# Kernel tuning notes

Measured on AMD Instinct MI355X. Metric: run time of the kernel, lower is better.

The kernel has to match this reference:

```python
import jax, jax.numpy as jnp
import numpy as np

LN_EPS = 1e-12
NEG_INF = -1e9


def setup_inputs() -> dict:
    key = jax.random.key(0)
    ks = jax.random.split(key, 4)
    B, S, H = 8, 2048, 1024
    inputs = jax.random.normal(ks[0], (B, S, H), dtype=jnp.float32)
    masks = jnp.ones((B, S), dtype=jnp.int32)
    scale = 1.0 / np.sqrt(H)
    Wq = jax.random.normal(ks[1], (H, H), dtype=jnp.float32) * scale
    bq = jnp.zeros((H,), dtype=jnp.float32)
    Wk = jax.random.normal(ks[2], (H, H), dtype=jnp.float32) * scale
    bk = jnp.zeros((H,), dtype=jnp.float32)
    ln_gamma = jnp.ones((H,), dtype=jnp.float32)
    ln_beta = jnp.zeros((H,), dtype=jnp.float32)
    return {"inputs": inputs, "masks": masks, "Wq": Wq, "bq": bq,
            "Wk": Wk, "bk": bk, "ln_gamma": ln_gamma, "ln_beta": ln_beta}


def _layernorm(x, gamma, beta):
    mu = jnp.mean(x, axis=-1, keepdims=True)
    var = jnp.mean(jnp.square(x - mu), axis=-1, keepdims=True)
    return (x - mu) * jax.lax.rsqrt(var + LN_EPS) * gamma + beta


def reference(inputs, masks, Wq, bq, Wk, bk, ln_gamma, ln_beta):
    # inputs: [B,S,H]; masks: [B,S] (1 = keep key position)
    H = inputs.shape[-1]
    query = inputs @ Wq + bq                      # [B,S,H]
    key_ = inputs @ Wk + bk                       # [B,S,H]
    scores = jnp.einsum('bqh,bkh->bqk', query, key_) * (1.0 / jnp.sqrt(jnp.float32(H)))
    # logits_mask: invalid key positions get large negative logit
    scores = jnp.where(masks[:, None, :] != 0, scores, NEG_INF)
    probs = jax.nn.softmax(scores, axis=-1)       # [B,S,S]
    context = jnp.einsum('bqk,bkh->bqh', probs, inputs)  # value = raw inputs
    return _layernorm(inputs + context, ln_gamma, ln_beta)
```

## Files before the change

kernel.cpp:

```cpp
#include <hip/hip_runtime.h>
#include <stdint.h>
#include <stddef.h>

typedef _Float16 f16_t;
typedef _Float16 f16x8 __attribute__((ext_vector_type(8)));
typedef _Float16 f16x4 __attribute__((ext_vector_type(4)));
typedef float    f32x4 __attribute__((ext_vector_type(4)));

#define AS_G __attribute__((address_space(1)))
#define AS_L __attribute__((address_space(3)))

__device__ __forceinline__ void gload_lds16(const void* g, void* l) {
  __builtin_amdgcn_global_load_lds((const AS_G uint32_t*)g, (AS_L uint32_t*)l, 16, 0, 0);
}

#define LN_EPS 1e-12f

__global__ __launch_bounds__(256) void cast_f16_kernel(const float* __restrict__ in,
                                                       f16_t* __restrict__ out) {
  int i = blockIdx.x * 256 + threadIdx.x;
  float4 v = ((const float4*)in)[i];
  f16x4 o = {(f16_t)v.x, (f16_t)v.y, (f16_t)v.z, (f16_t)v.w};
  ((f16x4*)out)[i] = o;
}

__global__ __launch_bounds__(256) void xprep_kernel(const float* __restrict__ in,
                                                    f16_t* __restrict__ xb,
                                                    f16_t* __restrict__ xt) {
  __shared__ float tile[32][33];
  int b = blockIdx.z;
  const float* inb = in + (size_t)b * 2048 * 1024;
  f16_t* xbb = xb + (size_t)b * 2048 * 1024;
  f16_t* xtb = xt + (size_t)b * 1024 * 2048;
  int tx = threadIdx.x, ty = threadIdx.y;
  int c0 = blockIdx.x * 32, r0 = blockIdx.y * 32;
#pragma unroll
  for (int i = 0; i < 32; i += 8) {
    float v = inb[(size_t)(r0 + ty + i) * 1024 + (c0 + tx)];
    tile[ty + i][tx] = v;
    xbb[(size_t)(r0 + ty + i) * 1024 + (c0 + tx)] = (f16_t)v;
  }
  __syncthreads();
#pragma unroll
  for (int i = 0; i < 32; i += 8)
    xtb[(size_t)(c0 + ty + i) * 2048 + (r0 + tx)] = (f16_t)tile[tx][ty + i];
}

__global__ __launch_bounds__(256) void wvec_kernel(const float* __restrict__ Wq,
                                                   const float* __restrict__ bq,
                                                   const float* __restrict__ Wk,
                                                   const float* __restrict__ bk,
                                                   float* __restrict__ wqbk,
                                                   float* __restrict__ wkbq,
                                                   float* __restrict__ c0) {
  __shared__ float red[4];
  int bid = blockIdx.x, tid = threadIdx.x;
  const float* rowp; const float* vecp; float* outp;
  if (bid < 1024)      { rowp = Wq + (size_t)bid * 1024; vecp = bk; outp = wqbk + bid; }
  else if (bid < 2048) { rowp = Wk + (size_t)(bid - 1024) * 1024; vecp = bq; outp = wkbq + (bid - 1024); }
  else                 { rowp = bq; vecp = bk; outp = c0; }
  float4 a = ((const float4*)rowp)[tid];
  float4 b = ((const float4*)vecp)[tid];
  float s = a.x * b.x + a.y * b.y + a.z * b.z + a.w * b.w;
#pragma unroll
  for (int off = 32; off > 0; off >>= 1) s += __shfl_xor(s, off, 64);
  if ((tid & 63) == 0) red[tid >> 6] = s;
  __syncthreads();
  if (tid == 0) *outp = red[0] + red[1] + red[2] + red[3];
}

__global__ __launch_bounds__(256) void cqck_kernel(const float* __restrict__ X,
                                                   const float* __restrict__ wqbk,
                                                   const float* __restrict__ wkbq,
                                                   float* __restrict__ cq,
                                                   float* __restrict__ ck) {
  __shared__ float r1[4], r2[4];
  int m = blockIdx.x, tid = threadIdx.x;
  float4 x = ((const float4*)(X + (size_t)m * 1024))[tid];
  float4 a = ((const float4*)wqbk)[tid];
  float4 b = ((const float4*)wkbq)[tid];
  float s1 = x.x * a.x + x.y * a.y + x.z * a.z + x.w * a.w;
  float s2 = x.x * b.x + x.y * b.y + x.z * b.z + x.w * b.w;
#pragma unroll
  for (int off = 32; off > 0; off >>= 1) { s1 += __shfl_xor(s1, off, 64); s2 += __shfl_xor(s2, off, 64); }
  if ((tid & 63) == 0) { r1[tid >> 6] = s1; r2[tid >> 6] = s2; }
  __syncthreads();
  if (tid == 0) {
    cq[m] = r1[0] + r1[1] + r1[2] + r1[3];
    ck[m] = r2[0] + r2[1] + r2[2] + r2[3];
  }
}

__global__ __launch_bounds__(256) void gemm_bt_kernel(
    const f16_t* __restrict__ A, const f16_t* __restrict__ Bt, f16_t* __restrict__ C,
    const float* __restrict__ cq, const float* __restrict__ ck, const float* __restrict__ c0p,
    const int* __restrict__ mask, const float* __restrict__ invl, float* __restrict__ lpart,
    int lda, int ldb, int ldc, int K, float scale, int mode,
    size_t sA, size_t sB, size_t sC) {
  __shared__ f16_t As[128 * 64];
  __shared__ f16_t Bs[128 * 64];

  const int tid = threadIdx.x;
  const int lane = tid & 63;
  const int wv = tid >> 6;
  const int m16 = lane & 15;
  const int quad = lane >> 4;
  const int wr = (wv >> 1) * 64;
  const int wc = (wv & 1) * 64;

  const f16_t* Ab = A + blockIdx.z * sA + (size_t)blockIdx.x * 128 * lda;
  const f16_t* Bb = Bt + blockIdx.z * sB + (size_t)blockIdx.y * 128 * ldb;

  const int lr8 = lane >> 3;
  const int ch8 = (lane & 7) ^ lr8;
  const f16_t* gA[4]; const f16_t* gB[4];
  f16_t* lA[4]; f16_t* lB[4];
#pragma unroll
  for (int j = 0; j < 4; ++j) {
    int row = wv * 32 + j * 8 + lr8;
    gA[j] = Ab + (size_t)row * lda + ch8 * 8;
    gB[j] = Bb + (size_t)row * ldb + ch8 * 8;
    lA[j] = &As[(wv * 32 + j * 8) * 64];
    lB[j] = &Bs[(wv * 32 + j * 8) * 64];
  }

  int aoff[4], boff[4], swz[2];
#pragma unroll
  for (int t = 0; t < 4; ++t) {
    aoff[t] = (wr + t * 16 + m16) * 64;
    boff[t] = (wc + t * 16 + m16) * 64;
  }
#pragma unroll
  for (int s = 0; s < 2; ++s)
    swz[s] = (((s << 2) | quad) ^ (m16 & 7)) * 8;

  f32x4 acc[4][4] = {};

  for (int k0 = 0; k0 < K; k0 += 64) {
#pragma unroll
    for (int j = 0; j < 4; ++j) {
      gload_lds16(gA[j] + k0, lA[j]);
      gload_lds16(gB[j] + k0, lB[j]);
    }
    __syncthreads();

#pragma unroll
    for (int s = 0; s < 2; ++s) {
      f16x8 af[4], bfr[4];
#pragma unroll
      for (int t = 0; t < 4; ++t) {
        af[t]  = *(const f16x8*)&As[aoff[t] + swz[s]];
        bfr[t] = *(const f16x8*)&Bs[boff[t] + swz[s]];
      }
#pragma unroll
      for (int rt = 0; rt < 4; ++rt)
#pragma unroll
        for (int ct = 0; ct < 4; ++ct)
          acc[rt][ct] = __builtin_amdgcn_mfma_f32_16x16x32_f16(af[rt], bfr[ct], acc[rt][ct], 0, 0, 0);
    }
    __syncthreads();
  }

  f16_t* Cb = C + blockIdx.z * sC;
  const int row0 = blockIdx.x * 128 + wr + quad * 4;
  const int col0 = blockIdx.y * 128 + wc + m16;
  if (mode == 0) {
#pragma unroll
    for (int ct = 0; ct < 4; ++ct)
#pragma unroll
      for (int rt = 0; rt < 4; ++rt)
#pragma unroll
        for (int r = 0; r < 4; ++r)
          Cb[(size_t)(row0 + rt * 16 + r) * ldc + col0 + ct * 16] = (f16_t)acc[rt][ct][r];
  } else if (mode == 1) {
    const int* mp = mask + blockIdx.z * 2048;
    const size_t rowg0 = blockIdx.z * 2048 + row0;
    const float c0 = *c0p;
    float rsum[4][4];
#pragma unroll
    for (int rt = 0; rt < 4; ++rt)
#pragma unroll
      for (int r = 0; r < 4; ++r) rsum[rt][r] = 0.f;
#pragma unroll
    for (int ct = 0; ct < 4; ++ct) {
      int col = col0 + ct * 16;
      bool keep = (mp[col] != 0);
      float ckv = ck[blockIdx.z * 2048 + col];
#pragma unroll
      for (int rt = 0; rt < 4; ++rt)
#pragma unroll
        for (int r = 0; r < 4; ++r) {
          float cqv = cq[rowg0 + rt * 16 + r];
          float p = keep ? __expf((acc[rt][ct][r] + cqv + ckv + c0) * scale) : 0.f;
          rsum[rt][r] += p;
          Cb[(size_t)(row0 + rt * 16 + r) * ldc + col] = (f16_t)p;
        }
    }
    const int chunk = blockIdx.y * 2 + (wv & 1);
#pragma unroll
    for (int rt = 0; rt < 4; ++rt)
#pragma unroll
      for (int r = 0; r < 4; ++r) {
        float v = rsum[rt][r];
        v += __shfl_xor(v, 1, 16);
        v += __shfl_xor(v, 2, 16);
        v += __shfl_xor(v, 4, 16);
        v += __shfl_xor(v, 8, 16);
        if (m16 == 0) lpart[(rowg0 + rt * 16 + r) * 32 + chunk] = v;
      }
  } else {
    const size_t rowg0 = blockIdx.z * 2048 + row0;
#pragma unroll
    for (int rt = 0; rt < 4; ++rt)
#pragma unroll
      for (int r = 0; r < 4; ++r) {
        float il = invl[rowg0 + rt * 16 + r];
#pragma unroll
        for (int ct = 0; ct < 4; ++ct)
          Cb[(size_t)(row0 + rt * 16 + r) * ldc + col0 + ct * 16] = (f16_t)(acc[rt][ct][r] * il);
      }
  }
}

__global__ __launch_bounds__(256) void lreduce_kernel(const float* __restrict__ lpart,
                                                      float* __restrict__ invl) {
  int m = blockIdx.x * 256 + threadIdx.x;
  const float4* p = (const float4*)(lpart + (size_t)m * 32);
  float s = 0.f;
#pragma unroll
  for (int j = 0; j < 8; ++j) {
    float4 v = p[j];
    s += v.x + v.y + v.z + v.w;
  }
  invl[m] = 1.0f / fmaxf(s, 1e-30f);
}

__global__ __launch_bounds__(256) void ln_kernel(const float* __restrict__ X,
                                                 const f16_t* __restrict__ Ctx,
                                                 const float* __restrict__ gamma,
                                                 const float* __restrict__ beta,
                                                 float* __restrict__ out) {
  __shared__ float r1[4], r2[4];
  const int tid = threadIdx.x;
  const size_t base = (size_t)blockIdx.x * 1024;
  float4 xv = ((const float4*)(X + base))[tid];
  f16x4 cv = ((const f16x4*)(Ctx + base))[tid];
  float v0 = xv.x + (float)cv[0];
  float v1 = xv.y + (float)cv[1];
  float v2 = xv.z + (float)cv[2];
  float v3 = xv.w + (float)cv[3];
  float s1 = v0 + v1 + v2 + v3;
  float s2 = v0 * v0 + v1 * v1 + v2 * v2 + v3 * v3;
#pragma unroll
  for (int off = 32; off > 0; off >>= 1) {
    s1 += __shfl_xor(s1, off, 64);
    s2 += __shfl_xor(s2, off, 64);
  }
  if ((tid & 63) == 0) { r1[tid >> 6] = s1; r2[tid >> 6] = s2; }
  __syncthreads();
  s1 = r1[0] + r1[1] + r1[2] + r1[3];
  s2 = r2[0] + r2[1] + r2[2] + r2[3];
  float mu = s1 * (1.0f / 1024.0f);
  float var = s2 * (1.0f / 1024.0f) - mu * mu;
  float rs = rsqrtf(fmaxf(var, 0.0f) + LN_EPS);
  float4 gv = ((const float4*)gamma)[tid];
  float4 bv = ((const float4*)beta)[tid];
  float4 o;
  o.x = (v0 - mu) * rs * gv.x + bv.x;
  o.y = (v1 - mu) * rs * gv.y + bv.y;
  o.z = (v2 - mu) * rs * gv.z + bv.z;
  o.w = (v3 - mu) * rs * gv.w + bv.w;
  ((float4*)(out + base))[tid] = o;
}

extern "C" void kernel_launch(void* const* d_in, const int* in_sizes, int n_in,
                              void* d_out, int out_size, void* d_ws, size_t ws_size,
                              hipStream_t stream) {
  const float* X     = (const float*)d_in[0];
  const int*   masks = (const int*)d_in[1];
  const float* Wq    = (const float*)d_in[2];
  const float* bq    = (const float*)d_in[3];
  const float* Wk    = (const float*)d_in[4];
  const float* bk    = (const float*)d_in[5];
  const float* gamma = (const float*)d_in[6];
  const float* beta  = (const float*)d_in[7];
  float* out = (float*)d_out;

  if (ws_size < 115343360u) return;
  char* ws = (char*)d_ws;
  f16_t* Xb   = (f16_t*)(ws + 0);
  f16_t* Xt   = (f16_t*)(ws + 33554432);
  f16_t* T    = (f16_t*)(ws + 67108864);
  f16_t* Wqf  = (f16_t*)(ws + 100663296);
  f16_t* Wkf  = (f16_t*)(ws + 102760448);
  f16_t* Wkq  = (f16_t*)(ws + 104857600);
  float* lpart= (float*)(ws + 106954752);
  float* cq   = (float*)(ws + 109051904);
  float* ck   = (float*)(ws + 109117440);
  float* invl = (float*)(ws + 109182976);
  float* wqbk = (float*)(ws + 109248512);
  float* wkbq = (float*)(ws + 109252608);
  float* c0   = (float*)(ws + 109256704);
  f16_t* Ctx  = Xb;
  f16_t* probs = (f16_t*)d_out;

  const size_t SH = 2048u * 1024u;
  const size_t SS = 2048u * 2048u;
  const size_t HS = 1024u * 2048u;

  xprep_kernel<<<dim3(32, 64, 8), dim3(32, 8), 0, stream>>>(X, Xb, Xt);
  cast_f16_kernel<<<1024, 256, 0, stream>>>(Wq, Wqf);
  cast_f16_kernel<<<1024, 256, 0, stream>>>(Wk, Wkf);
  wvec_kernel<<<2049, 256, 0, stream>>>(Wq, bq, Wk, bk, wqbk, wkbq, c0);
  cqck_kernel<<<16384, 256, 0, stream>>>(X, wqbk, wkbq, cq, ck);

  gemm_bt_kernel<<<dim3(8, 8, 1), 256, 0, stream>>>(
      Wkf, Wqf, Wkq, nullptr, nullptr, nullptr, nullptr, nullptr, nullptr,
      1024, 1024, 1024, 1024, 0.f, 0, 0, 0, 0);

  gemm_bt_kernel<<<dim3(128, 8, 1), 256, 0, stream>>>(
      Xb, Wkq, T, nullptr, nullptr, nullptr, nullptr, nullptr, nullptr,
      1024, 1024, 1024, 1024, 0.f, 0, 0, 0, 0);

  gemm_bt_kernel<<<dim3(16, 16, 8), 256, 0, stream>>>(
      T, Xb, probs, cq, ck, c0, masks, nullptr, lpart,
      1024, 1024, 2048, 1024, 0.03125f, 1, SH, SH, SS);

  lreduce_kernel<<<64, 256, 0, stream>>>(lpart, invl);

  gemm_bt_kernel<<<dim3(16, 8, 8), 256, 0, stream>>>(
      probs, Xt, Ctx, nullptr, nullptr, nullptr, nullptr, invl, nullptr,
      2048, 2048, 1024, 2048, 0.f, 2, SS, HS, SH);

  ln_kernel<<<16384, 256, 0, stream>>>(X, Ctx, gamma, beta, out);
}
```

Before: 479.2 us.

## Warp-specialize GEMM with producer waves and a four-stage LDS ring

Restructures the shared GEMM kernel so that two extra waves act as producers, issuing global-to-LDS loads into a 4-slot ring buffer three K-steps ahead. The four consumer waves only read LDS and issue MFMAs, synchronised by raw s_barrier and explicit vmcnt waits. The K-step drops from 64 to 32 with a new swizzle. This aims to hide global load latency that the old load-sync-compute-sync loop exposed, at the cost of more LDS per block (64KB), which may reduce occupancy, plus fragile hand-written waitcnt logic.

```diff
diff --git a/kernel.cpp b/kernel.cpp
--- a/kernel.cpp
+++ b/kernel.cpp
@@ -10,7 +10,7 @@
 #define AS_G __attribute__((address_space(1)))
 #define AS_L __attribute__((address_space(3)))
 
-__device__ __forceinline__ void gload_lds16(const void* g, void* l) {
+__device__ __forceinline__ void gload_lds16(const void* g, AS_L void* l) {
   __builtin_amdgcn_global_load_lds((const AS_G uint32_t*)g, (AS_L uint32_t*)l, 16, 0, 0);
 }
 
@@ -91,75 +91,90 @@
   }
 }
 
-__global__ __launch_bounds__(256) void gemm_bt_kernel(
+__global__ __launch_bounds__(384) void gemm_bt_kernel(
     const f16_t* __restrict__ A, const f16_t* __restrict__ Bt, f16_t* __restrict__ C,
     const float* __restrict__ cq, const float* __restrict__ ck, const float* __restrict__ c0p,
     const int* __restrict__ mask, const float* __restrict__ invl, float* __restrict__ lpart,
     int lda, int ldb, int ldc, int K, float scale, int mode,
     size_t sA, size_t sB, size_t sC) {
-  __shared__ f16_t As[128 * 64];
-  __shared__ f16_t Bs[128 * 64];
+  __shared__ f16_t ring[4 * 8192];
 
   const int tid = threadIdx.x;
   const int lane = tid & 63;
   const int wv = tid >> 6;
   const int m16 = lane & 15;
   const int quad = lane >> 4;
+  const int nk = K >> 5;
+
+  const f16_t* Ab = A + blockIdx.z * sA + (size_t)blockIdx.x * 128 * lda;
+  const f16_t* Bb = Bt + blockIdx.z * sB + (size_t)blockIdx.y * 128 * ldb;
+
+  const int ch8 = ((lane & 3) ^ ((lane >> 3) & 3)) * 8;
+  const int prow = lane >> 2;
+
   const int wr = (wv >> 1) * 64;
   const int wc = (wv & 1) * 64;
-
-  const f16_t* Ab = A + blockIdx.z * sA + (size_t)blockIdx.x * 128 * lda;
-  const f16_t* Bb = Bt + blockIdx.z * sB + (size_t)blockIdx.y * 128 * ldb;
-
-  const int lr8 = lane >> 3;
-  const int ch8 = (lane & 7) ^ lr8;
-  const f16_t* gA[4]; const f16_t* gB[4];
-  f16_t* lA[4]; f16_t* lB[4];
-#pragma unroll
-  for (int j = 0; j < 4; ++j) {
-    int row = wv * 32 + j * 8 + lr8;
-    gA[j] = Ab + (size_t)row * lda + ch8 * 8;
-    gB[j] = Bb + (size_t)row * ldb + ch8 * 8;
-    lA[j] = &As[(wv * 32 + j * 8) * 64];
-    lB[j] = &Bs[(wv * 32 + j * 8) * 64];
-  }
-
-  int aoff[4], boff[4], swz[2];
-#pragma unroll
-  for (int t = 0; t < 4; ++t) {
-    aoff[t] = (wr + t * 16 + m16) * 64;
-    boff[t] = (wc + t * 16 + m16) * 64;
-  }
-#pragma unroll
-  for (int s = 0; s < 2; ++s)
-    swz[s] = (((s << 2) | quad) ^ (m16 & 7)) * 8;
+  const int eslot8 = (quad ^ ((m16 >> 1) & 3)) * 8;
+  const AS_L f16_t* pa = (const AS_L f16_t*)ring + (wr + m16) * 32 + eslot8;
+  const AS_L f16_t* pb = (const AS_L f16_t*)ring + 4096 + (wc + m16) * 32 + eslot8;
 
   f32x4 acc[4][4] = {};
 
-  for (int k0 = 0; k0 < K; k0 += 64) {
-#pragma unroll
-    for (int j = 0; j < 4; ++j) {
-      gload_lds16(gA[j] + k0, lA[j]);
-      gload_lds16(gB[j] + k0, lB[j]);
+  if (wv >= 4) {
+    const int ab = wv - 4;
+    const f16_t* g = (ab ? Bb : Ab) + (size_t)prow * (ab ? ldb : lda) + ch8;
+    const int ld = ab ? ldb : lda;
+    AS_L f16_t* l0 = (AS_L f16_t*)ring + ab * 4096;
+#pragma unroll
+    for (int s = 0; s < 3; ++s)
+#pragma unroll
+      for (int j = 0; j < 8; ++j)
+        gload_lds16(g + (size_t)(j * 16) * ld + s * 32, l0 + s * 8192 + j * 512);
+  }
+
+  for (int t4 = 0; t4 < nk; t4 += 4) {
+#pragma unroll
+    for (int s = 0; s < 4; ++s) {
+      const int t = t4 + s;
+      if (wv >= 4) {
+        if (t < nk - 2)       asm volatile("s_waitcnt vmcnt(16)" ::: "memory");
+        else if (t == nk - 2) asm volatile("s_waitcnt vmcnt(8)" ::: "memory");
+        else                  asm volatile("s_waitcnt vmcnt(0)" ::: "memory");
+      }
+      asm volatile("s_barrier" ::: "memory");
+      if (wv < 4) {
+        f16x8 a0, a1, a2, a3, b0, b1, b2, b3;
+        asm volatile("ds_read_b128 %0, %1 offset:%c2" : "=v"(a0) : "v"(pa), "i"(s * 16384 + 0 * 1024));
+        asm volatile("ds_read_b128 %0, %1 offset:%c2" : "=v"(a1) : "v"(pa), "i"(s * 16384 + 1 * 1024));
+        asm volatile("ds_read_b128 %0, %1 offset:%c2" : "=v"(a2) : "v"(pa), "i"(s * 16384 + 2 * 1024));
+        asm volatile("ds_read_b128 %0, %1 offset:%c2" : "=v"(a3) : "v"(pa), "i"(s * 16384 + 3 * 1024));
+        asm volatile("ds_read_b128 %0, %1 offset:%c2" : "=v"(b0) : "v"(pb), "i"(s * 16384 + 0 * 1024));
+        asm volatile("ds_read_b128 %0, %1 offset:%c2" : "=v"(b1) : "v"(pb), "i"(s * 16384 + 1 * 1024));
+        asm volatile("ds_read_b128 %0, %1 offset:%c2" : "=v"(b2) : "v"(pb), "i"(s * 16384 + 2 * 1024));
+        asm volatile("ds_read_b128 %0, %1 offset:%c2" : "=v"(b3) : "v"(pb), "i"(s * 16384 + 3 * 1024));
+        asm volatile("s_waitcnt lgkmcnt(0)"
+                     : "+v"(a0), "+v"(a1), "+v"(a2), "+v"(a3),
+                       "+v"(b0), "+v"(b1), "+v"(b2), "+v"(b3) :: "memory");
+        f16x8 af[4] = {a0, a1, a2, a3}, bf[4] = {b0, b1, b2, b3};
+#pragma unroll
+        for (int rt = 0; rt < 4; ++rt)
+#pragma unroll
+          for (int ct = 0; ct < 4; ++ct)
+            acc[rt][ct] = __builtin_amdgcn_mfma_f32_16x16x32_f16(af[rt], bf[ct], acc[rt][ct], 0, 0, 0);
+      } else if (t + 3 < nk) {
+        const int sl = (s + 3) & 3;
+        const int ab = wv - 4;
+        const f16_t* g = (ab ? Bb : Ab) + (size_t)prow * (ab ? ldb : lda) + ch8;
+        const int ld = ab ? ldb : lda;
+        AS_L f16_t* l0 = (AS_L f16_t*)ring + ab * 4096;
+#pragma unroll
+        for (int j = 0; j < 8; ++j)
+          gload_lds16(g + (size_t)(j * 16) * ld + (t + 3) * 32, l0 + sl * 8192 + j * 512);
+      }
     }
-    __syncthreads();
-
-#pragma unroll
-    for (int s = 0; s < 2; ++s) {
-      f16x8 af[4], bfr[4];
-#pragma unroll
-      for (int t = 0; t < 4; ++t) {
-        af[t]  = *(const f16x8*)&As[aoff[t] + swz[s]];
-        bfr[t] = *(const f16x8*)&Bs[boff[t] + swz[s]];
-      }
-#pragma unroll
-      for (int rt = 0; rt < 4; ++rt)
-#pragma unroll
-        for (int ct = 0; ct < 4; ++ct)
-          acc[rt][ct] = __builtin_amdgcn_mfma_f32_16x16x32_f16(af[rt], bfr[ct], acc[rt][ct], 0, 0, 0);
-    }
-    __syncthreads();
-  }
+  }
+
+  if (wv >= 4) return;
 
   f16_t* Cb = C + blockIdx.z * sC;
   const int row0 = blockIdx.x * 128 + wr + quad * 4;
@@ -314,21 +329,21 @@
   wvec_kernel<<<2049, 256, 0, stream>>>(Wq, bq, Wk, bk, wqbk, wkbq, c0);
   cqck_kernel<<<16384, 256, 0, stream>>>(X, wqbk, wkbq, cq, ck);
 
-  gemm_bt_kernel<<<dim3(8, 8, 1), 256, 0, stream>>>(
+  gemm_bt_kernel<<<dim3(8, 8, 1), 384, 0, stream>>>(
       Wkf, Wqf, Wkq, nullptr, nullptr, nullptr, nullptr, nullptr, nullptr,
       1024, 1024, 1024, 1024, 0.f, 0, 0, 0, 0);
 
-  gemm_bt_kernel<<<dim3(128, 8, 1), 256, 0, stream>>>(
+  gemm_bt_kernel<<<dim3(128, 8, 1), 384, 0, stream>>>(
       Xb, Wkq, T, nullptr, nullptr, nullptr, nullptr, nullptr, nullptr,
       1024, 1024, 1024, 1024, 0.f, 0, 0, 0, 0);
 
-  gemm_bt_kernel<<<dim3(16, 16, 8), 256, 0, stream>>>(
+  gemm_bt_kernel<<<dim3(16, 16, 8), 384, 0, stream>>>(
       T, Xb, probs, cq, ck, c0, masks, nullptr, lpart,
       1024, 1024, 2048, 1024, 0.03125f, 1, SH, SH, SS);
 
   lreduce_kernel<<<64, 256, 0, stream>>>(lpart, invl);
 
-  gemm_bt_kernel<<<dim3(16, 8, 8), 256, 0, stream>>>(
+  gemm_bt_kernel<<<dim3(16, 8, 8), 384, 0, stream>>>(
       probs, Xt, Ctx, nullptr, nullptr, nullptr, nullptr, invl, nullptr,
       2048, 2048, 1024, 2048, 0.f, 2, SS, HS, SH);
 
```

New measurement: 528.2 us. 10.2% more time.
